# Kernel optimization log

Measured on AMD Instinct MI355X. Metric: run time of the kernel, lower is better.

## Reference

```python
import jax, jax.numpy as jnp
import numpy as np

EMBED_DIM = 1024
NUM_HEADS = 16
HEAD_DIM = EMBED_DIM // NUM_HEADS


def setup_inputs() -> dict:
    key = jax.random.key(0)
    ks = jax.random.split(key, 12)
    B, Nq, Nkv, D = 4, 1024, 1024, EMBED_DIM
    s = 1.0 / np.sqrt(D)
    return {
        "query": jax.random.normal(ks[0], (B, Nq, D), jnp.float32),
        "key_value": jax.random.normal(ks[1], (B, Nkv, D), jnp.float32),
        "Wq": jax.random.normal(ks[2], (D, D), jnp.float32) * s,
        "bq": jnp.zeros((D,), jnp.float32),
        "Wk": jax.random.normal(ks[3], (D, D), jnp.float32) * s,
        "bk": jnp.zeros((D,), jnp.float32),
        "Wv": jax.random.normal(ks[4], (D, D), jnp.float32) * s,
        "bv": jnp.zeros((D,), jnp.float32),
        "Wo": jax.random.normal(ks[5], (D, D), jnp.float32) * s,
        "bo": jnp.zeros((D,), jnp.float32),
        "gamma": jnp.ones((D,), jnp.float32),
        "beta": jnp.zeros((D,), jnp.float32),
    }


def reference(query, key_value, Wq, bq, Wk, bk, Wv, bv, Wo, bo, gamma, beta):
    B, Nq, D = query.shape
    Nkv = key_value.shape[1]
    H, Hd = NUM_HEADS, HEAD_DIM
    # projections -> [B, H, N, Hd]
    q = (query @ Wq + bq).reshape(B, Nq, H, Hd).transpose(0, 2, 1, 3)
    k = (key_value @ Wk + bk).reshape(B, Nkv, H, Hd).transpose(0, 2, 1, 3)
    v = (key_value @ Wv + bv).reshape(B, Nkv, H, Hd).transpose(0, 2, 1, 3)
    scores = jnp.einsum("bhqd,bhkd->bhqk", q, k) / jnp.sqrt(jnp.float32(Hd))
    attn = jax.nn.softmax(scores, axis=-1)  # dropout = identity at eval
    out = jnp.einsum("bhqk,bhkd->bhqd", attn, v)
    out = out.transpose(0, 2, 1, 3).reshape(B, Nq, D)
    out = out @ Wo + bo
    # residual + LayerNorm (eps = 1e-5, torch default)
    x = query + out
    mu = jnp.mean(x, axis=-1, keepdims=True)
    var = jnp.mean(jnp.square(x - mu), axis=-1, keepdims=True)
    return (x - mu) / jnp.sqrt(var + 1e-5) * gamma + beta
```

## Files before the change

### kernel.cpp

```cpp
#include <hip/hip_runtime.h>

typedef unsigned short u16;
typedef unsigned int u32;
typedef __attribute__((ext_vector_type(4))) unsigned short u16x4;
typedef __attribute__((ext_vector_type(8))) short short8;
typedef __attribute__((ext_vector_type(4))) float f32x4;

#define MFMA16(a, b, c) __builtin_amdgcn_mfma_f32_16x16x32_bf16(a, b, c, 0, 0, 0)

__device__ __forceinline__ u16 f2bf(float f) {
  unsigned u = __builtin_bit_cast(unsigned, f);
  u += 0x7fffu + ((u >> 16) & 1u);
  return (u16)(u >> 16);
}

__device__ __forceinline__ u32 cvtpk(float lo, float hi) {
  u32 r;
  asm("v_cvt_pk_bf16_f32 %0, %1, %2" : "=v"(r) : "v"(lo), "v"(hi));
  return r;
}

__device__ __forceinline__ float ex2(float x) {
  float r;
  asm("v_exp_f32 %0, %1" : "=v"(r) : "v"(x));
  return r;
}

__device__ __forceinline__ void gl_lds16(const void* g, void* l) {
  __builtin_amdgcn_global_load_lds((const __attribute__((address_space(1))) char*)g,
                                   (__attribute__((address_space(3))) char*)l, 16, 0, 0);
}

__global__ __launch_bounds__(256) void cvt_bf16_k(const float* __restrict__ in,
                                                  u16* __restrict__ out) {
  int i = blockIdx.x * 256 + threadIdx.x;
  float4 v = ((const float4*)in)[i];
  u16x4 o;
  o.x = f2bf(v.x); o.y = f2bf(v.y); o.z = f2bf(v.z); o.w = f2bf(v.w);
  ((u16x4*)out)[i] = o;
}

__global__ __launch_bounds__(256) void wt_k(const float* __restrict__ W0, const float* __restrict__ W1,
                                            const float* __restrict__ W2, const float* __restrict__ W3,
                                            u16* __restrict__ T0, u16* __restrict__ T1,
                                            u16* __restrict__ T2, u16* __restrict__ T3) {
  const float* W; u16* T;
  switch (blockIdx.z) {
    case 0: W = W0; T = T0; break;
    case 1: W = W1; T = T1; break;
    case 2: W = W2; T = T2; break;
    default: W = W3; T = T3; break;
  }
  __shared__ __align__(16) u16 t[64][72];
  const int k0 = blockIdx.y * 64, n0 = blockIdx.x * 64;
  const int tid = threadIdx.x;
  const int r = tid >> 4, c4 = (tid & 15) * 4;
#pragma unroll
  for (int i = 0; i < 4; i++) {
    float4 v = *(const float4*)(W + (k0 + r + i * 16) * 1024 + n0 + c4);
    u16x4 o;
    o.x = f2bf(v.x); o.y = f2bf(v.y); o.z = f2bf(v.z); o.w = f2bf(v.w);
    *(u16x4*)&t[r + i * 16][c4] = o;
  }
  __syncthreads();
#pragma unroll
  for (int i = 0; i < 4; i++) {
    int nr = r + i * 16;
    u16x4 o;
    o.x = t[c4 + 0][nr]; o.y = t[c4 + 1][nr]; o.z = t[c4 + 2][nr]; o.w = t[c4 + 3][nr];
    *(u16x4*)(T + (n0 + nr) * 1024 + k0 + c4) = o;
  }
}

__global__ __launch_bounds__(256, 3) void gemmqkv_k(
    const u16* __restrict__ qbf, const u16* __restrict__ kvbf,
    const u16* __restrict__ Wqt, const u16* __restrict__ Wkt, const u16* __restrict__ Wvt,
    const float* __restrict__ pbq, const float* __restrict__ pbk, const float* __restrict__ pbv,
    u16* __restrict__ Qh, u16* __restrict__ Kh, u16* __restrict__ Vth) {
  const int lin = blockIdx.x;
  const int swz = (lin & 7) * 96 + (lin >> 3);
  const int x = swz & 7, y = (swz >> 3) & 31, z = swz >> 8;

  const u16* A  = (z == 0) ? qbf : kvbf;
  const u16* Bt = (z == 0) ? Wqt : (z == 1 ? Wkt : Wvt);
  const float* bias = (z == 0) ? pbq : (z == 1 ? pbk : pbv);

  __shared__ __align__(16) u16 As[128 * 32];
  __shared__ __align__(16) u16 Bs[128 * 32];
  const int tid = threadIdx.x;
  const int l = tid & 63, w = tid >> 6;
  const int lr = l >> 4, lc = l & 15;
  const int wr = w >> 1, wc = w & 1;
  const int m0 = y * 128, n0 = x * 128;

  f32x4 acc[4][4] = {};

  const int sr = tid >> 2, sc = (tid & 3) * 8;
  const u16* Ag = A + (m0 + sr) * 1024 + sc;
  const u16* Bg = Bt + (n0 + sr) * 1024 + sc;
  u16* AsW = As + tid * 8;
  u16* BsW = Bs + tid * 8;

  for (int k0 = 0; k0 < 1024; k0 += 32) {
    __syncthreads();
    gl_lds16(Ag + k0, AsW);
    gl_lds16(Ag + 64 * 1024 + k0, AsW + 2048);
    gl_lds16(Bg + k0, BsW);
    gl_lds16(Bg + 64 * 1024 + k0, BsW + 2048);
    __syncthreads();
    const u16* PA = (z == 2) ? Bs : As;
    const u16* PB = (z == 2) ? As : Bs;
    short8 af[4], bf[4];
    const int ks8 = lr * 8;
#pragma unroll
    for (int m = 0; m < 4; m++)
      af[m] = *(const short8*)(PA + (wr * 64 + m * 16 + lc) * 32 + ks8);
#pragma unroll
    for (int n = 0; n < 4; n++)
      bf[n] = *(const short8*)(PB + (wc * 64 + n * 16 + lc) * 32 + ks8);
#pragma unroll
    for (int m = 0; m < 4; m++)
#pragma unroll
      for (int n = 0; n < 4; n++)
        acc[m][n] = MFMA16(af[m], bf[n], acc[m][n]);
  }

  if (z == 2) {
#pragma unroll
    for (int m = 0; m < 4; m++) {
#pragma unroll
      for (int r = 0; r < 4; r++) {
        int ncol = n0 + wr * 64 + m * 16 + lr * 4 + r;
        float bb = bias[ncol];
        int h = ncol >> 6, d = ncol & 63;
#pragma unroll
        for (int n = 0; n < 4; n++) {
          int tok = m0 + wc * 64 + n * 16 + lc;
          Vth[(((tok >> 10) * 16 + h) * 64 + d) * 1024 + (tok & 1023)] =
              f2bf(acc[m][n][r] + bb);
        }
      }
    }
  } else {
    u16* outb = (z == 0) ? Qh : Kh;
    const float scale = (z == 0) ? 0.18033688f : 1.0f;
#pragma unroll
    for (int m = 0; m < 4; m++)
#pragma unroll
      for (int n = 0; n < 4; n++) {
        int ncol = n0 + wc * 64 + n * 16 + lc;
        float bb = bias[ncol];
        int h = ncol >> 6, d = ncol & 63;
#pragma unroll
        for (int r = 0; r < 4; r++) {
          int tok = m0 + wr * 64 + m * 16 + lr * 4 + r;
          outb[(((tok >> 10) * 16 + h) * 1024 + (tok & 1023)) * 64 + d] =
              f2bf((acc[m][n][r] + bb) * scale);
        }
      }
  }
}

__global__ __launch_bounds__(256, 4) void gemmo_k(const u16* __restrict__ A,
                                                  const u16* __restrict__ Bt,
                                                  const float* __restrict__ bias,
                                                  float* __restrict__ outf) {
  const int lin = blockIdx.x;
  const int swz = (lin & 7) * 64 + (lin >> 3);
  const int x = swz & 15, y = swz >> 4;

  __shared__ __align__(16) u16 As[128 * 32];
  __shared__ __align__(16) u16 Bs[64 * 32];
  const int tid = threadIdx.x;
  const int l = tid & 63, w = tid >> 6;
  const int lr = l >> 4, lc = l & 15;
  const int wr = w >> 1, wc = w & 1;
  const int m0 = y * 128, n0 = x * 64;

  f32x4 acc[4][2] = {};
  const int sc = (tid & 3) * 8;
  const u16* Ag = A + (m0 + (tid >> 2)) * 1024 + sc;
  const u16* Bg = Bt + (n0 + (tid >> 2)) * 1024 + sc;

  for (int k0 = 0; k0 < 1024; k0 += 32) {
    __syncthreads();
    gl_lds16(Ag + k0, As + tid * 8);
    gl_lds16(Ag + 64 * 1024 + k0, As + 2048 + tid * 8);
    gl_lds16(Bg + k0, Bs + tid * 8);
    __syncthreads();
    short8 af[4], bf[2];
    const int ks8 = lr * 8;
#pragma unroll
    for (int m = 0; m < 4; m++)
      af[m] = *(const short8*)(As + (wr * 64 + m * 16 + lc) * 32 + ks8);
#pragma unroll
    for (int n = 0; n < 2; n++)
      bf[n] = *(const short8*)(Bs + (wc * 32 + n * 16 + lc) * 32 + ks8);
#pragma unroll
    for (int m = 0; m < 4; m++)
#pragma unroll
      for (int n = 0; n < 2; n++)
        acc[m][n] = MFMA16(af[m], bf[n], acc[m][n]);
  }
#pragma unroll
  for (int m = 0; m < 4; m++)
#pragma unroll
    for (int n = 0; n < 2; n++) {
      int ncol = n0 + wc * 32 + n * 16 + lc;
      float bb = bias[ncol];
#pragma unroll
      for (int r = 0; r < 4; r++) {
        int tok = m0 + wr * 64 + m * 16 + lr * 4 + r;
        outf[tok * 1024 + ncol] = acc[m][n][r] + bb;
      }
    }
}

__global__ __launch_bounds__(256, 3) void attn_k(const u16* __restrict__ Q,
                                                 const u16* __restrict__ K,
                                                 const u16* __restrict__ Vt,
                                                 u16* __restrict__ O) {
  const int bid = blockIdx.x;
  const int xcd = bid & 7, j = bid >> 3;
  const int bh = xcd + 8 * (j & 7);
  const int q0 = (j >> 3) * 64;
  const int tid = threadIdx.x;
  const int w = tid >> 6, l = tid & 63;
  const int lr = l >> 4, lc = l & 15;
  const u16* Qh = Q + bh * (1024 * 64);
  const u16* Kh = K + bh * (1024 * 64);
  const u16* Vh = Vt + bh * (64 * 1024);

  __shared__ __align__(16) u16 Ks[2][64 * 64];
  __shared__ __align__(16) u16 Vs[2][64 * 64];
  __shared__ __align__(16) u32 Plds[4][16][36];

  const int st_row = tid >> 3;
  const int st_cb = (tid & 7) * 16;
  const int sw1 = (st_cb ^ ((st_row & 7) << 4)) >> 1;
  const int st_row2 = st_row + 32;
  const int sw2 = (st_cb ^ ((st_row2 & 7) << 4)) >> 1;

  short8 bq[2];
#pragma unroll
  for (int ks = 0; ks < 2; ks++)
    bq[ks] = *(const short8*)(Qh + (q0 + w * 16 + lc) * 64 + ks * 32 + lr * 8);

  f32x4 oacc[4] = {};
  float mrun = -1e30f, lrun = 0.f;

  gl_lds16(Kh + st_row * 64 + sw1, &Ks[0][tid * 8]);
  gl_lds16(Kh + st_row2 * 64 + sw2, &Ks[0][2048 + tid * 8]);
  gl_lds16(Vh + st_row * 1024 + sw1, &Vs[0][tid * 8]);
  gl_lds16(Vh + st_row2 * 1024 + sw2, &Vs[0][2048 + tid * 8]);

  for (int t = 0; t < 16; ++t) {
    const int pb = t & 1;
    if (t < 15) {
      const int kvn = (t + 1) * 64;
      gl_lds16(Kh + (kvn + st_row) * 64 + sw1, &Ks[pb ^ 1][tid * 8]);
      gl_lds16(Kh + (kvn + st_row2) * 64 + sw2, &Ks[pb ^ 1][2048 + tid * 8]);
      gl_lds16(Vh + st_row * 1024 + kvn + sw1, &Vs[pb ^ 1][tid * 8]);
      gl_lds16(Vh + st_row2 * 1024 + kvn + sw2, &Vs[pb ^ 1][2048 + tid * 8]);
      asm volatile("s_waitcnt vmcnt(4)" ::: "memory");
    } else {
      asm volatile("s_waitcnt vmcnt(0)" ::: "memory");
    }
    __builtin_amdgcn_s_barrier();
    asm volatile("" ::: "memory");

    const u16* Kb = Ks[pb];
    const u16* Vb = Vs[pb];

    f32x4 s[4] = {};
    __builtin_amdgcn_s_setprio(1);
#pragma unroll
    for (int mk = 0; mk < 4; mk++) {
      const int krow = mk * 16 + lc;
      const u16* kp = Kb + krow * 64;
#pragma unroll
      for (int ks = 0; ks < 2; ks++) {
        const int cb = (ks * 64 + lr * 16) ^ ((krow & 7) << 4);
        short8 ak = *(const short8*)(kp + (cb >> 1));
        s[mk] = MFMA16(ak, bq[ks], s[mk]);
      }
    }
    __builtin_amdgcn_s_setprio(0);

    float mx;
    {
      float a = fmaxf(fmaxf(s[0][0], s[0][1]), fmaxf(s[0][2], s[0][3]));
      float b = fmaxf(fmaxf(s[1][0], s[1][1]), fmaxf(s[1][2], s[1][3]));
      float c = fmaxf(fmaxf(s[2][0], s[2][1]), fmaxf(s[2][2], s[2][3]));
      float d = fmaxf(fmaxf(s[3][0], s[3][1]), fmaxf(s[3][2], s[3][3]));
      mx = fmaxf(fmaxf(a, b), fmaxf(c, d));
    }
    mx = fmaxf(mx, __shfl_xor(mx, 16));
    mx = fmaxf(mx, __shfl_xor(mx, 32));

    if (!__all(mx <= mrun + 8.f)) {
      float mnew = fmaxf(mrun, mx);
      float alpha = ex2(mrun - mnew);
      mrun = mnew;
      lrun *= alpha;
      float alr[4];
#pragma unroll
      for (int r = 0; r < 4; r++) alr[r] = __shfl(alpha, lr * 4 + r);
#pragma unroll
      for (int nd = 0; nd < 4; nd++)
#pragma unroll
        for (int r = 0; r < 4; r++) oacc[nd][r] *= alr[r];
    }

#pragma unroll
    for (int mk = 0; mk < 4; mk++)
#pragma unroll
      for (int r = 0; r < 4; r++) s[mk][r] = ex2(s[mk][r] - mrun);
    float ps;
    {
      float a = (s[0][0] + s[0][1]) + (s[0][2] + s[0][3]);
      float b = (s[1][0] + s[1][1]) + (s[1][2] + s[1][3]);
      float c = (s[2][0] + s[2][1]) + (s[2][2] + s[2][3]);
      float d = (s[3][0] + s[3][1]) + (s[3][2] + s[3][3]);
      ps = (a + b) + (c + d);
    }
    ps += __shfl_xor(ps, 16);
    ps += __shfl_xor(ps, 32);
    lrun += ps;

    u32* PW = &Plds[w][lc][0];
#pragma unroll
    for (int mk = 0; mk < 4; mk++)
#pragma unroll
      for (int rr = 0; rr < 2; rr++)
        PW[mk * 8 + lr * 2 + rr] = cvtpk(s[mk][2 * rr], s[mk][2 * rr + 1]);

    __builtin_amdgcn_s_setprio(1);
#pragma unroll
    for (int ks = 0; ks < 2; ks++) {
      short8 ap = *(const short8*)&Plds[w][lc][ks * 16 + lr * 4];
#pragma unroll
      for (int nd = 0; nd < 4; nd++) {
        const int vrow = nd * 16 + lc;
        const int cb = (ks * 64 + lr * 16) ^ ((vrow & 7) << 4);
        short8 bv = *(const short8*)(Vb + vrow * 64 + (cb >> 1));
        oacc[nd] = MFMA16(ap, bv, oacc[nd]);
      }
    }
    __builtin_amdgcn_s_setprio(0);

    asm volatile("" ::: "memory");
    __builtin_amdgcn_s_barrier();
  }

  float inv = 1.f / lrun;
  float invr[4];
#pragma unroll
  for (int r = 0; r < 4; r++) invr[r] = __shfl(inv, lr * 4 + r);
  const int b = bh >> 4, h = bh & 15;
#pragma unroll
  for (int r = 0; r < 4; r++) {
    int row = b * 1024 + q0 + w * 16 + lr * 4 + r;
#pragma unroll
    for (int nd = 0; nd < 4; nd++)
      O[row * 1024 + h * 64 + nd * 16 + lc] = f2bf(oacc[nd][r] * invr[r]);
  }
}

__global__ __launch_bounds__(256) void ln_k(const float* __restrict__ q,
                                            const float* __restrict__ p2,
                                            const float* __restrict__ gamma,
                                            const float* __restrict__ beta,
                                            float* __restrict__ out) {
  const int row = blockIdx.x, tid = threadIdx.x;
  float4 xq = ((const float4*)(q + row * 1024))[tid];
  float4 xp = ((const float4*)(p2 + row * 1024))[tid];
  float4 x = {xq.x + xp.x, xq.y + xp.y, xq.z + xp.z, xq.w + xp.w};
  float s = x.x + x.y + x.z + x.w;
#pragma unroll
  for (int off = 1; off < 64; off <<= 1) s += __shfl_xor(s, off);
  __shared__ float red[8];
  const int w = tid >> 6;
  if ((tid & 63) == 0) red[w] = s;
  __syncthreads();
  float mu = (red[0] + red[1] + red[2] + red[3]) * (1.0f / 1024.0f);
  float4 dx = {x.x - mu, x.y - mu, x.z - mu, x.w - mu};
  float s2 = dx.x * dx.x + dx.y * dx.y + dx.z * dx.z + dx.w * dx.w;
#pragma unroll
  for (int off = 1; off < 64; off <<= 1) s2 += __shfl_xor(s2, off);
  if ((tid & 63) == 0) red[4 + w] = s2;
  __syncthreads();
  float var = (red[4] + red[5] + red[6] + red[7]) * (1.0f / 1024.0f);
  float rs = rsqrtf(var + 1e-5f);
  float4 g = ((const float4*)gamma)[tid];
  float4 bb = ((const float4*)beta)[tid];
  float4 o = {dx.x * rs * g.x + bb.x, dx.y * rs * g.y + bb.y,
              dx.z * rs * g.z + bb.z, dx.w * rs * g.w + bb.w};
  ((float4*)(out + row * 1024))[tid] = o;
}

extern "C" void kernel_launch(void* const* d_in, const int* in_sizes, int n_in,
                              void* d_out, int out_size, void* d_ws, size_t ws_size,
                              hipStream_t stream) {
  const float* query = (const float*)d_in[0];
  const float* kv    = (const float*)d_in[1];
  const float* Wq = (const float*)d_in[2];
  const float* bq = (const float*)d_in[3];
  const float* Wk = (const float*)d_in[4];
  const float* bk = (const float*)d_in[5];
  const float* Wv = (const float*)d_in[6];
  const float* bv = (const float*)d_in[7];
  const float* Wo = (const float*)d_in[8];
  const float* bo = (const float*)d_in[9];
  const float* gamma = (const float*)d_in[10];
  const float* beta  = (const float*)d_in[11];
  float* out = (float*)d_out;

  char* ws = (char*)d_ws;
  const size_t MB = 1u << 20;
  u16* qbf  = (u16*)(ws + 0 * MB);
  u16* kvbf = (u16*)(ws + 8 * MB);
  u16* Wqt  = (u16*)(ws + 16 * MB);
  u16* Wkt  = (u16*)(ws + 18 * MB);
  u16* Wvt  = (u16*)(ws + 20 * MB);
  u16* Wot  = (u16*)(ws + 22 * MB);
  u16* Qh   = (u16*)(ws + 24 * MB);
  u16* Kh   = (u16*)(ws + 32 * MB);
  u16* Vth  = (u16*)(ws + 40 * MB);
  u16* attO = (u16*)(ws + 48 * MB);
  float* p2 = (float*)(ws + 56 * MB);

  cvt_bf16_k<<<dim3(4096), dim3(256), 0, stream>>>(query, qbf);
  cvt_bf16_k<<<dim3(4096), dim3(256), 0, stream>>>(kv, kvbf);
  wt_k<<<dim3(16, 16, 4), dim3(256), 0, stream>>>(Wq, Wk, Wv, Wo, Wqt, Wkt, Wvt, Wot);

  gemmqkv_k<<<dim3(768), dim3(256), 0, stream>>>(qbf, kvbf, Wqt, Wkt, Wvt,
                                                 bq, bk, bv, Qh, Kh, Vth);

  attn_k<<<dim3(1024), dim3(256), 0, stream>>>(Qh, Kh, Vth, attO);

  gemmo_k<<<dim3(512), dim3(256), 0, stream>>>(attO, Wot, bo, p2);

  ln_k<<<dim3(4096), dim3(256), 0, stream>>>(query, p2, gamma, beta, out);
}
```

Measured before the change: 123.1 us.

## Double K-step in QKV GEMM, raise attention occupancy, XOR-swizzle P LDS buffer

```diff
diff --git a/kernel.cpp b/kernel.cpp
--- a/kernel.cpp
+++ b/kernel.cpp
@@ -85,8 +85,8 @@
   const u16* Bt = (z == 0) ? Wqt : (z == 1 ? Wkt : Wvt);
   const float* bias = (z == 0) ? pbq : (z == 1 ? pbk : pbv);
 
-  __shared__ __align__(16) u16 As[128 * 32];
-  __shared__ __align__(16) u16 Bs[128 * 32];
+  __shared__ __align__(16) u16 As[128 * 64];
+  __shared__ __align__(16) u16 Bs[128 * 64];
   const int tid = threadIdx.x;
   const int l = tid & 63, w = tid >> 6;
   const int lr = l >> 4, lc = l & 15;
@@ -98,31 +98,39 @@
   const int sr = tid >> 2, sc = (tid & 3) * 8;
   const u16* Ag = A + (m0 + sr) * 1024 + sc;
   const u16* Bg = Bt + (n0 + sr) * 1024 + sc;
-  u16* AsW = As + tid * 8;
-  u16* BsW = Bs + tid * 8;
-
-  for (int k0 = 0; k0 < 1024; k0 += 32) {
+
+  for (int k0 = 0; k0 < 1024; k0 += 64) {
     __syncthreads();
-    gl_lds16(Ag + k0, AsW);
-    gl_lds16(Ag + 64 * 1024 + k0, AsW + 2048);
-    gl_lds16(Bg + k0, BsW);
-    gl_lds16(Bg + 64 * 1024 + k0, BsW + 2048);
+    gl_lds16(Ag + k0, As + tid * 8);
+    gl_lds16(Ag + 64 * 1024 + k0, As + 2048 + tid * 8);
+    gl_lds16(Bg + k0, Bs + tid * 8);
+    gl_lds16(Bg + 64 * 1024 + k0, Bs + 2048 + tid * 8);
+    gl_lds16(Ag + k0 + 32, As + 4096 + tid * 8);
+    gl_lds16(Ag + 64 * 1024 + k0 + 32, As + 6144 + tid * 8);
+    gl_lds16(Bg + k0 + 32, Bs + 4096 + tid * 8);
+    gl_lds16(Bg + 64 * 1024 + k0 + 32, Bs + 6144 + tid * 8);
     __syncthreads();
     const u16* PA = (z == 2) ? Bs : As;
     const u16* PB = (z == 2) ? As : Bs;
-    short8 af[4], bf[4];
+    short8 af[4][2], bf[4][2];
     const int ks8 = lr * 8;
 #pragma unroll
     for (int m = 0; m < 4; m++)
-      af[m] = *(const short8*)(PA + (wr * 64 + m * 16 + lc) * 32 + ks8);
+#pragma unroll
+      for (int h = 0; h < 2; h++)
+        af[m][h] = *(const short8*)(PA + h * 4096 + (wr * 64 + m * 16 + lc) * 32 + ks8);
 #pragma unroll
     for (int n = 0; n < 4; n++)
-      bf[n] = *(const short8*)(PB + (wc * 64 + n * 16 + lc) * 32 + ks8);
+#pragma unroll
+      for (int h = 0; h < 2; h++)
+        bf[n][h] = *(const short8*)(PB + h * 4096 + (wc * 64 + n * 16 + lc) * 32 + ks8);
 #pragma unroll
     for (int m = 0; m < 4; m++)
 #pragma unroll
-      for (int n = 0; n < 4; n++)
-        acc[m][n] = MFMA16(af[m], bf[n], acc[m][n]);
+      for (int n = 0; n < 4; n++) {
+        acc[m][n] = MFMA16(af[m][0], bf[n][0], acc[m][n]);
+        acc[m][n] = MFMA16(af[m][1], bf[n][1], acc[m][n]);
+      }
   }
 
   if (z == 2) {
@@ -216,7 +224,7 @@
     }
 }
 
-__global__ __launch_bounds__(256, 3) void attn_k(const u16* __restrict__ Q,
+__global__ __launch_bounds__(256, 4) void attn_k(const u16* __restrict__ Q,
                                                  const u16* __restrict__ K,
                                                  const u16* __restrict__ Vt,
                                                  u16* __restrict__ O) {
@@ -233,7 +241,7 @@
 
   __shared__ __align__(16) u16 Ks[2][64 * 64];
   __shared__ __align__(16) u16 Vs[2][64 * 64];
-  __shared__ __align__(16) u32 Plds[4][16][36];
+  __shared__ __align__(16) u32 Plds[4][16][32];
 
   const int st_row = tid >> 3;
   const int st_cb = (tid & 7) * 16;
@@ -253,6 +261,8 @@
   gl_lds16(Kh + st_row2 * 64 + sw2, &Ks[0][2048 + tid * 8]);
   gl_lds16(Vh + st_row * 1024 + sw1, &Vs[0][tid * 8]);
   gl_lds16(Vh + st_row2 * 1024 + sw2, &Vs[0][2048 + tid * 8]);
+
+  const int xw = (lc & 7) << 2;
 
   for (int t = 0; t < 16; ++t) {
     const int pb = t & 1;
@@ -333,12 +343,12 @@
     for (int mk = 0; mk < 4; mk++)
 #pragma unroll
       for (int rr = 0; rr < 2; rr++)
-        PW[mk * 8 + lr * 2 + rr] = cvtpk(s[mk][2 * rr], s[mk][2 * rr + 1]);
+        PW[(mk * 8 + lr * 2 + rr) ^ xw] = cvtpk(s[mk][2 * rr], s[mk][2 * rr + 1]);
 
     __builtin_amdgcn_s_setprio(1);
 #pragma unroll
     for (int ks = 0; ks < 2; ks++) {
-      short8 ap = *(const short8*)&Plds[w][lc][ks * 16 + lr * 4];
+      short8 ap = *(const short8*)&Plds[w][lc][(ks * 16 + lr * 4) ^ xw];
 #pragma unroll
       for (int nd = 0; nd < 4; nd++) {
         const int vrow = nd * 16 + lc;
```

Measured after the change: 113.0 us. 1.09x faster.
